# Performance work log

Measured on AMD Instinct MI355X. Metric: run time of the kernel, lower is better.

The kernel has to match this reference:

```python
import jax, jax.numpy as jnp
import numpy as np

B, N, F_IN, F_OUT = 8, 8192, 128, 128
E = 1_048_576
BN = B * N


def setup_inputs() -> dict:
    key = jax.random.key(0)
    ks = jax.random.split(key, 9)
    glorot = (6.0 / (F_IN + F_OUT)) ** 0.5
    return {
        "X": jax.random.normal(ks[0], (B, N, F_IN), dtype=jnp.float32),
        "W0": jax.random.uniform(ks[1], (F_IN, F_OUT), jnp.float32, -glorot, glorot),
        "W1": jax.random.uniform(ks[2], (F_IN, F_OUT), jnp.float32, -glorot, glorot),
        "rows0": jax.random.randint(ks[3], (E,), 0, BN, dtype=jnp.int32),
        "cols0": jax.random.randint(ks[4], (E,), 0, BN, dtype=jnp.int32),
        "vals0": jax.random.uniform(ks[5], (E,), dtype=jnp.float32),
        "rows1": jax.random.randint(ks[6], (E,), 0, BN, dtype=jnp.int32),
        "cols1": jax.random.randint(ks[7], (E,), 0, BN, dtype=jnp.int32),
        "vals1": jax.random.uniform(ks[8], (E,), dtype=jnp.float32),
    }


def _spmm(rows, cols, vals, H, n):
    # COO sparse [n, n] @ dense H [n, F]: gather source rows, scale, scatter-add.
    return jax.ops.segment_sum(vals[:, None] * H[cols], rows, num_segments=n)


def reference(X, W0, W1, rows0, cols0, vals0, rows1, cols1, vals1):
    b, n, f_in = X.shape
    X2 = X.reshape(-1, f_in)                      # [B*N, F_in]
    h0 = _spmm(rows0, cols0, vals0, X2 @ W0, b * n)  # filter_0 @ (X W0)
    h1 = _spmm(rows1, cols1, vals1, X2 @ W1, b * n)  # filter_1 @ (X W1)
    out = jax.nn.relu(h0 + h1).reshape(b, n, -1)  # add_n + relu
    return out
```

## Files before the change

kernel.cpp:

```cpp
#include <hip/hip_runtime.h>


typedef unsigned int   uint;
typedef unsigned short ushort;
typedef unsigned char  uchar;
typedef float f32x4 __attribute__((ext_vector_type(4)));
typedef int   i32x4 __attribute__((ext_vector_type(4)));

constexpr int NB  = 256;
constexpr int EPB = 8192;
constexpr int CAP = 8192;

__device__ __forceinline__ ushort f2bf(float f) {
    uint u = __float_as_uint(f);
    u += 0x7fffu + ((u >> 16) & 1u);
    return (ushort)(u >> 16);
}
__device__ __forceinline__ float bf2f(ushort h) {
    return __uint_as_float((uint)h << 16);
}

#define ACC_FENCE(a) asm volatile("s_nop 7\n\ts_nop 7" : "+v"(a))

__global__ __launch_bounds__(64) void w_swz(const float* __restrict__ W0,
                                            const float* __restrict__ W1,
                                            uint4* __restrict__ Wswz) {
    const int bx = blockIdx.x;
    const int f  = bx >> 5;
    const int ct = (bx >> 2) & 7;
    const int kt = bx & 3;
    const int l  = threadIdx.x;
    const float* W = f ? W1 : W0;
    const int kbase = kt * 32 + (l >> 4) * 8;
    const int col   = ct * 16 + (l & 15);
    ushort h[8];
#pragma unroll
    for (int j = 0; j < 8; ++j)
        h[j] = f2bf(W[(kbase + j) * 128 + col]);
    uint4 o;
    o.x = (uint)h[0] | ((uint)h[1] << 16);
    o.y = (uint)h[2] | ((uint)h[3] << 16);
    o.z = (uint)h[4] | ((uint)h[5] << 16);
    o.w = (uint)h[6] | ((uint)h[7] << 16);
    Wswz[((f * 8 + ct) * 4 + kt) * 64 + l] = o;
}

__global__ __launch_bounds__(256) void gemm_mfma(const float* __restrict__ X,
                                                 const i32x4* __restrict__ Wswz,
                                                 ushort* __restrict__ H, int BN) {
    __shared__ ushort xs_hi[64][136];
    __shared__ ushort xs_lo[64][136];
    const int tid = threadIdx.x;
    const int l = tid & 63;
    const int w = tid >> 6;
    const long rbase = (long)blockIdx.x * 64;

    const float4* Xv = reinterpret_cast<const float4*>(X + rbase * 128);
#pragma unroll
    for (int i = 0; i < 8; ++i) {
        int idx = i * 256 + tid;
        int row = idx >> 5, c4 = idx & 31;
        float4 v = Xv[idx];
        ushort4 hi, lo;
        hi.x = f2bf(v.x); lo.x = f2bf(v.x - bf2f(hi.x));
        hi.y = f2bf(v.y); lo.y = f2bf(v.y - bf2f(hi.y));
        hi.z = f2bf(v.z); lo.z = f2bf(v.z - bf2f(hi.z));
        hi.w = f2bf(v.w); lo.w = f2bf(v.w - bf2f(hi.w));
        *reinterpret_cast<ushort4*>(&xs_hi[row][c4 * 4]) = hi;
        *reinterpret_cast<ushort4*>(&xs_lo[row][c4 * 4]) = lo;
    }
    __syncthreads();

    i32x4 a_hi[4], a_lo[4];
    const int arow = w * 16 + (l & 15);
    const int kb = (l >> 4) * 8;
#pragma unroll
    for (int kt = 0; kt < 4; ++kt) {
        a_hi[kt] = *reinterpret_cast<const i32x4*>(&xs_hi[arow][kt * 32 + kb]);
        a_lo[kt] = *reinterpret_cast<const i32x4*>(&xs_lo[arow][kt * 32 + kb]);
    }

    f32x4 acc[2][8];
#pragma unroll
    for (int f = 0; f < 2; ++f)
#pragma unroll
        for (int ct = 0; ct < 8; ++ct)
            acc[f][ct] = (f32x4)0.0f;

#pragma unroll
    for (int ct = 0; ct < 8; ++ct)
#pragma unroll
        for (int f = 0; f < 2; ++f)
#pragma unroll
            for (int kt = 0; kt < 4; ++kt) {
                i32x4 b = Wswz[((f * 8 + ct) * 4 + kt) * 64 + l];
                asm volatile("v_mfma_f32_16x16x32_bf16 %0, %1, %2, %0"
                             : "+v"(acc[f][ct]) : "v"(a_hi[kt]), "v"(b));
                asm volatile("v_mfma_f32_16x16x32_bf16 %0, %1, %2, %0"
                             : "+v"(acc[f][ct]) : "v"(a_lo[kt]), "v"(b));
            }

#pragma unroll
    for (int ct = 0; ct < 8; ++ct)
#pragma unroll
        for (int f = 0; f < 2; ++f) {
            f32x4 a = acc[f][ct];
            ACC_FENCE(a);
            ushort* Hf = H + (size_t)f * BN * 128;
            size_t base = (size_t)(rbase + w * 16 + (l >> 4) * 4) * 128
                        + ct * 16 + (l & 15);
            Hf[base]       = f2bf(a.x);
            Hf[base + 128] = f2bf(a.y);
            Hf[base + 256] = f2bf(a.z);
            Hf[base + 384] = f2bf(a.w);
        }
}

__global__ __launch_bounds__(256) void hist_coarse(const int* __restrict__ r0,
                                                   const int* __restrict__ r1,
                                                   int* __restrict__ cnt, int E) {
    __shared__ int h[NB];
    const int f = blockIdx.y, t = threadIdx.x;
    const int* rows = f ? r1 : r0;
    h[t] = 0;
    __syncthreads();
    const int base = blockIdx.x * EPB;
    for (int k = 0; k < EPB / 256; ++k) {
        int e = base + k * 256 + t;
        if (e < E) atomicAdd(&h[rows[e] >> 8], 1);
    }
    __syncthreads();
    if (h[t]) atomicAdd(&cnt[f * NB + t], h[t]);
}

__global__ __launch_bounds__(256) void scan_coarse(const int* __restrict__ cnt,
                                                   int* __restrict__ bbase,
                                                   int* __restrict__ bcur) {
    __shared__ int s[NB];
    const int f = blockIdx.x, t = threadIdx.x;
    int v = cnt[f * NB + t];
    s[t] = v;
    __syncthreads();
    for (int off = 1; off < NB; off <<= 1) {
        int u = (t >= off) ? s[t - off] : 0;
        __syncthreads();
        s[t] += u;
        __syncthreads();
    }
    int base = s[t] - v;
    bbase[f * NB + t] = base;
    bcur [f * NB + t] = base;
}

__global__ __launch_bounds__(256) void partition(const int* __restrict__ r0,
                                                 const int* __restrict__ c0,
                                                 const float* __restrict__ v0,
                                                 const int* __restrict__ r1,
                                                 const int* __restrict__ c1,
                                                 const float* __restrict__ v1,
                                                 int* __restrict__ bcur,
                                                 uint* __restrict__ cvy,
                                                 uchar* __restrict__ cvr, int E) {
    __shared__ int h[NB];
    __shared__ int cur[NB];
    const int f = blockIdx.y, t = threadIdx.x;
    const int*   rows = f ? r1 : r0;
    const int*   cols = f ? c1 : c0;
    const float* vals = f ? v1 : v0;
    const int base = blockIdx.x * EPB;

    h[t] = 0;
    __syncthreads();
    for (int k = 0; k < EPB / 256; ++k) {
        int e = base + k * 256 + t;
        if (e < E) atomicAdd(&h[rows[e] >> 8], 1);
    }
    __syncthreads();
    cur[t] = atomicAdd(&bcur[f * NB + t], h[t]);
    __syncthreads();

    uint*  yout = cvy + (size_t)f * E;
    uchar* rout = cvr + (size_t)f * E;
    for (int k = 0; k < EPB / 256; ++k) {
        int e = base + k * 256 + t;
        if (e < E) {
            int r = rows[e];
            int pos = atomicAdd(&cur[r >> 8], 1);
            yout[pos] = ((uint)cols[e] << 16) | (uint)f2bf(vals[e]);
            rout[pos] = (uchar)(r & 255);
        }
    }
}

__device__ __forceinline__ void fma4(float4& a, float v, ushort4 h) {
    a.x = fmaf(v, bf2f(h.x), a.x);
    a.y = fmaf(v, bf2f(h.y), a.y);
    a.z = fmaf(v, bf2f(h.z), a.z);
    a.w = fmaf(v, bf2f(h.w), a.w);
}

__global__ __launch_bounds__(1024) void sort_gather(
        const uint* __restrict__ cvy, const uchar* __restrict__ cvr,
        const int* __restrict__ bbase, const int* __restrict__ bcur,
        const ushort* __restrict__ H, int BN,
        float* __restrict__ out, int E) {
    __shared__ uint cvl[2][CAP];
    __shared__ int rp[2][NB + 1];
    __shared__ int hcnt[NB];
    __shared__ int curs[NB];
    __shared__ int sstart[2], scount[2], sovf[2];

    const int b = blockIdx.x;
    const int t = threadIdx.x;

#pragma unroll 1
    for (int f = 0; f < 2; ++f) {
        if (t == 0) {
            int s0 = bbase[f * NB + b];
            int e0 = bcur [f * NB + b];
            sstart[f] = s0;
            scount[f] = e0 - s0;
            sovf[f]   = (e0 - s0) > CAP;
        }
        if (t < NB) hcnt[t] = 0;
        __syncthreads();
        const int s = sstart[f], n = scount[f];
        const uchar* rin = cvr + (size_t)f * E + s;
        const uint*  yin = cvy + (size_t)f * E + s;
        for (int i = t; i < n; i += 1024)
            atomicAdd(&hcnt[rin[i]], 1);
        __syncthreads();
        int v = (t < NB) ? hcnt[t] : 0;
        if (t < NB) curs[t] = v;
        __syncthreads();
        for (int off = 1; off < NB; off <<= 1) {
            int u = 0;
            if (t < NB && t >= off) u = curs[t - off];
            __syncthreads();
            if (t < NB) curs[t] += u;
            __syncthreads();
        }
        if (t < NB) {
            int ex = curs[t] - v;
            rp[f][t] = ex;
            curs[t] = ex;
        }
        if (t == 0) rp[f][NB] = n;
        __syncthreads();
        if (!sovf[f]) {
            for (int i = t; i < n; i += 1024) {
                uchar r = rin[i];
                int pos = atomicAdd(&curs[r], 1);
                cvl[f][pos] = __builtin_nontemporal_load(&yin[i]);
            }
        }
        __syncthreads();
    }

    const int half = t >> 5;
    const int sub  = t & 31;
    f32x4* outv = reinterpret_cast<f32x4*>(out);

#pragma unroll 1
    for (int k = 0; k < 8; ++k) {
        const int lr = k * 32 + half;
        const long gr = (long)b * NB + lr;

        float4 a0 = make_float4(0.f, 0.f, 0.f, 0.f);
        float4 a1 = make_float4(0.f, 0.f, 0.f, 0.f);
        float4 a2 = make_float4(0.f, 0.f, 0.f, 0.f);
        float4 a3 = make_float4(0.f, 0.f, 0.f, 0.f);

#pragma unroll
        for (int f = 0; f < 2; ++f) {
            const ushort* Hf = H + (size_t)f * BN * 128;
            if (!sovf[f]) {
                int e = rp[f][lr];
                const int e1 = rp[f][lr + 1];
                for (; e + 7 < e1; e += 8) {
                    uint p0 = cvl[f][e],     p1 = cvl[f][e + 1];
                    uint p2 = cvl[f][e + 2], p3 = cvl[f][e + 3];
                    uint p4 = cvl[f][e + 4], p5 = cvl[f][e + 5];
                    uint p6 = cvl[f][e + 6], p7 = cvl[f][e + 7];
                    ushort4 h0 = reinterpret_cast<const ushort4*>(Hf + (size_t)(p0 >> 16) * 128)[sub];
                    ushort4 h1 = reinterpret_cast<const ushort4*>(Hf + (size_t)(p1 >> 16) * 128)[sub];
                    ushort4 h2 = reinterpret_cast<const ushort4*>(Hf + (size_t)(p2 >> 16) * 128)[sub];
                    ushort4 h3 = reinterpret_cast<const ushort4*>(Hf + (size_t)(p3 >> 16) * 128)[sub];
                    ushort4 h4 = reinterpret_cast<const ushort4*>(Hf + (size_t)(p4 >> 16) * 128)[sub];
                    ushort4 h5 = reinterpret_cast<const ushort4*>(Hf + (size_t)(p5 >> 16) * 128)[sub];
                    ushort4 h6 = reinterpret_cast<const ushort4*>(Hf + (size_t)(p6 >> 16) * 128)[sub];
                    ushort4 h7 = reinterpret_cast<const ushort4*>(Hf + (size_t)(p7 >> 16) * 128)[sub];
                    fma4(a0, __uint_as_float(p0 << 16), h0);
                    fma4(a1, __uint_as_float(p1 << 16), h1);
                    fma4(a2, __uint_as_float(p2 << 16), h2);
                    fma4(a3, __uint_as_float(p3 << 16), h3);
                    fma4(a0, __uint_as_float(p4 << 16), h4);
                    fma4(a1, __uint_as_float(p5 << 16), h5);
                    fma4(a2, __uint_as_float(p6 << 16), h6);
                    fma4(a3, __uint_as_float(p7 << 16), h7);
                }
                for (; e + 3 < e1; e += 4) {
                    uint p0 = cvl[f][e],     p1 = cvl[f][e + 1];
                    uint p2 = cvl[f][e + 2], p3 = cvl[f][e + 3];
                    ushort4 h0 = reinterpret_cast<const ushort4*>(Hf + (size_t)(p0 >> 16) * 128)[sub];
                    ushort4 h1 = reinterpret_cast<const ushort4*>(Hf + (size_t)(p1 >> 16) * 128)[sub];
                    ushort4 h2 = reinterpret_cast<const ushort4*>(Hf + (size_t)(p2 >> 16) * 128)[sub];
                    ushort4 h3 = reinterpret_cast<const ushort4*>(Hf + (size_t)(p3 >> 16) * 128)[sub];
                    fma4(a0, __uint_as_float(p0 << 16), h0);
                    fma4(a1, __uint_as_float(p1 << 16), h1);
                    fma4(a2, __uint_as_float(p2 << 16), h2);
                    fma4(a3, __uint_as_float(p3 << 16), h3);
                }
                for (; e < e1; ++e) {
                    uint p0 = cvl[f][e];
                    ushort4 h0 = reinterpret_cast<const ushort4*>(Hf + (size_t)(p0 >> 16) * 128)[sub];
                    fma4(a0, __uint_as_float(p0 << 16), h0);
                }
            } else {
                const int s = sstart[f], n = scount[f];
                const uchar* rin = cvr + (size_t)f * E + s;
                const uint*  yin = cvy + (size_t)f * E + s;
                for (int i = 0; i < n; ++i) {
                    if (rin[i] == (uchar)lr) {
                        uint p0 = yin[i];
                        ushort4 h0 = reinterpret_cast<const ushort4*>(Hf + (size_t)(p0 >> 16) * 128)[sub];
                        fma4(a0, __uint_as_float(p0 << 16), h0);
                    }
                }
            }
        }

        f32x4 o;
        o.x = fmaxf((a0.x + a1.x) + (a2.x + a3.x), 0.0f);
        o.y = fmaxf((a0.y + a1.y) + (a2.y + a3.y), 0.0f);
        o.z = fmaxf((a0.z + a1.z) + (a2.z + a3.z), 0.0f);
        o.w = fmaxf((a0.w + a1.w) + (a2.w + a3.w), 0.0f);
        __builtin_nontemporal_store(o, outv + gr * 32 + sub);
    }
}

extern "C" void kernel_launch(void* const* d_in, const int* in_sizes, int n_in,
                              void* d_out, int out_size, void* d_ws, size_t ws_size,
                              hipStream_t stream) {
    const float* X     = (const float*)d_in[0];
    const float* W0    = (const float*)d_in[1];
    const float* W1    = (const float*)d_in[2];
    const int*   rows0 = (const int*)d_in[3];
    const int*   cols0 = (const int*)d_in[4];
    const float* vals0 = (const float*)d_in[5];
    const int*   rows1 = (const int*)d_in[6];
    const int*   cols1 = (const int*)d_in[7];
    const float* vals1 = (const float*)d_in[8];
    float* out = (float*)d_out;

    const int BN = in_sizes[0] / 128;
    const int E  = in_sizes[3];
    const int partb = (E + EPB - 1) / EPB;

    char* ws = (char*)d_ws;
    size_t off = 0;
    auto alloc = [&](size_t bytes) {
        void* p = ws + off;
        off = (off + bytes + 255) & ~(size_t)255;
        return p;
    };
    ushort* H     = (ushort*)alloc((size_t)2 * BN * 128 * sizeof(ushort));
    uint4*  Wswz  = (uint4*) alloc((size_t)2 * 128 * 128 * sizeof(ushort));
    uint*   cvy   = (uint*)  alloc((size_t)2 * E * sizeof(uint));
    uchar*  cvr   = (uchar*) alloc((size_t)2 * E * sizeof(uchar));
    int*    cnt   = (int*)   alloc((size_t)2 * NB * sizeof(int));
    int*    bbase = (int*)   alloc((size_t)2 * NB * sizeof(int));
    int*    bcur  = (int*)   alloc((size_t)2 * NB * sizeof(int));

    w_swz<<<64, 64, 0, stream>>>(W0, W1, Wswz);
    gemm_mfma<<<BN / 64, 256, 0, stream>>>(X, (const i32x4*)Wswz, H, BN);

    hipMemsetAsync(cnt, 0, (size_t)2 * NB * sizeof(int), stream);
    hist_coarse<<<dim3(partb, 2), 256, 0, stream>>>(rows0, rows1, cnt, E);
    scan_coarse<<<2, 256, 0, stream>>>(cnt, bbase, bcur);
    partition<<<dim3(partb, 2), 256, 0, stream>>>(rows0, cols0, vals0,
                                                  rows1, cols1, vals1,
                                                  bcur, cvy, cvr, E);
    sort_gather<<<NB, 1024, 0, stream>>>(cvy, cvr, bbase, bcur, H, BN, out, E);
}
```

Before: 166.9 us.

## Double coarse buckets to 512, shrink per-block LDS, fold counter zeroing into w_swz

Splits rows into 512 coarse buckets of 128 rows instead of 256 buckets of 256 rows. The sort_gather kernel then runs 512 blocks with a smaller LDS edge buffer, aiming for more blocks in flight and better occupancy across CUs. Partition blocks now process 16384 edges each, and the histogram memset is folded into an extra block of the w_swz kernel to save one launch. The risk is that CAP=3072 sits close to the expected ~2048 edges per bucket, so any overflow drops to the slow path.

Result: slower. 202.3 us, median of 2 (+21.2%).

```diff
diff --git a/kernel.cpp b/kernel.cpp
--- a/kernel.cpp
+++ b/kernel.cpp
@@ -7,9 +7,10 @@
 typedef float f32x4 __attribute__((ext_vector_type(4)));
 typedef int   i32x4 __attribute__((ext_vector_type(4)));
 
-constexpr int NB  = 256;
-constexpr int EPB = 8192;
-constexpr int CAP = 8192;
+constexpr int NBK = 512;
+constexpr int RPB = 128;
+constexpr int EPB = 16384;
+constexpr int CAP = 3072;
 
 __device__ __forceinline__ ushort f2bf(float f) {
     uint u = __float_as_uint(f);
@@ -24,12 +25,17 @@
 
 __global__ __launch_bounds__(64) void w_swz(const float* __restrict__ W0,
                                             const float* __restrict__ W1,
-                                            uint4* __restrict__ Wswz) {
+                                            uint4* __restrict__ Wswz,
+                                            int* __restrict__ cnt) {
     const int bx = blockIdx.x;
+    const int l  = threadIdx.x;
+    if (bx == 64) {
+        for (int i = l; i < 2 * NBK; i += 64) cnt[i] = 0;
+        return;
+    }
     const int f  = bx >> 5;
     const int ct = (bx >> 2) & 7;
     const int kt = bx & 3;
-    const int l  = threadIdx.x;
     const float* W = f ? W1 : W0;
     const int kbase = kt * 32 + (l >> 4) * 8;
     const int col   = ct * 16 + (l & 15);
@@ -119,37 +125,38 @@
 __global__ __launch_bounds__(256) void hist_coarse(const int* __restrict__ r0,
                                                    const int* __restrict__ r1,
                                                    int* __restrict__ cnt, int E) {
-    __shared__ int h[NB];
+    __shared__ int h[NBK];
     const int f = blockIdx.y, t = threadIdx.x;
     const int* rows = f ? r1 : r0;
-    h[t] = 0;
+    for (int i = t; i < NBK; i += 256) h[i] = 0;
     __syncthreads();
     const int base = blockIdx.x * EPB;
     for (int k = 0; k < EPB / 256; ++k) {
         int e = base + k * 256 + t;
-        if (e < E) atomicAdd(&h[rows[e] >> 8], 1);
-    }
-    __syncthreads();
-    if (h[t]) atomicAdd(&cnt[f * NB + t], h[t]);
-}
-
-__global__ __launch_bounds__(256) void scan_coarse(const int* __restrict__ cnt,
+        if (e < E) atomicAdd(&h[rows[e] >> 7], 1);
+    }
+    __syncthreads();
+    for (int i = t; i < NBK; i += 256)
+        if (h[i]) atomicAdd(&cnt[f * NBK + i], h[i]);
+}
+
+__global__ __launch_bounds__(512) void scan_coarse(const int* __restrict__ cnt,
                                                    int* __restrict__ bbase,
                                                    int* __restrict__ bcur) {
-    __shared__ int s[NB];
+    __shared__ int s[NBK];
     const int f = blockIdx.x, t = threadIdx.x;
-    int v = cnt[f * NB + t];
+    int v = cnt[f * NBK + t];
     s[t] = v;
     __syncthreads();
-    for (int off = 1; off < NB; off <<= 1) {
+    for (int off = 1; off < NBK; off <<= 1) {
         int u = (t >= off) ? s[t - off] : 0;
         __syncthreads();
         s[t] += u;
         __syncthreads();
     }
     int base = s[t] - v;
-    bbase[f * NB + t] = base;
-    bcur [f * NB + t] = base;
+    bbase[f * NBK + t] = base;
+    bcur [f * NBK + t] = base;
 }
 
 __global__ __launch_bounds__(256) void partition(const int* __restrict__ r0,
@@ -161,22 +168,23 @@
                                                  int* __restrict__ bcur,
                                                  uint* __restrict__ cvy,
                                                  uchar* __restrict__ cvr, int E) {
-    __shared__ int h[NB];
-    __shared__ int cur[NB];
+    __shared__ int h[NBK];
+    __shared__ int cur[NBK];
     const int f = blockIdx.y, t = threadIdx.x;
     const int*   rows = f ? r1 : r0;
     const int*   cols = f ? c1 : c0;
     const float* vals = f ? v1 : v0;
     const int base = blockIdx.x * EPB;
 
-    h[t] = 0;
+    for (int i = t; i < NBK; i += 256) h[i] = 0;
     __syncthreads();
     for (int k = 0; k < EPB / 256; ++k) {
         int e = base + k * 256 + t;
-        if (e < E) atomicAdd(&h[rows[e] >> 8], 1);
-    }
-    __syncthreads();
-    cur[t] = atomicAdd(&bcur[f * NB + t], h[t]);
+        if (e < E) atomicAdd(&h[rows[e] >> 7], 1);
+    }
+    __syncthreads();
+    for (int i = t; i < NBK; i += 256)
+        cur[i] = atomicAdd(&bcur[f * NBK + i], h[i]);
     __syncthreads();
 
     uint*  yout = cvy + (size_t)f * E;
@@ -185,9 +193,9 @@
         int e = base + k * 256 + t;
         if (e < E) {
             int r = rows[e];
-            int pos = atomicAdd(&cur[r >> 8], 1);
+            int pos = atomicAdd(&cur[r >> 7], 1);
             yout[pos] = ((uint)cols[e] << 16) | (uint)f2bf(vals[e]);
-            rout[pos] = (uchar)(r & 255);
+            rout[pos] = (uchar)(r & 127);
         }
     }
 }
@@ -205,9 +213,9 @@
         const ushort* __restrict__ H, int BN,
         float* __restrict__ out, int E) {
     __shared__ uint cvl[2][CAP];
-    __shared__ int rp[2][NB + 1];
-    __shared__ int hcnt[NB];
-    __shared__ int curs[NB];
+    __shared__ int rp[2][RPB + 1];
+    __shared__ int hcnt[RPB];
+    __shared__ int curs[RPB];
     __shared__ int sstart[2], scount[2], sovf[2];
 
     const int b = blockIdx.x;
@@ -216,13 +224,13 @@
 #pragma unroll 1
     for (int f = 0; f < 2; ++f) {
         if (t == 0) {
-            int s0 = bbase[f * NB + b];
-            int e0 = bcur [f * NB + b];
+            int s0 = bbase[f * NBK + b];
+            int e0 = bcur [f * NBK + b];
             sstart[f] = s0;
             scount[f] = e0 - s0;
             sovf[f]   = (e0 - s0) > CAP;
         }
-        if (t < NB) hcnt[t] = 0;
+        if (t < RPB) hcnt[t] = 0;
         __syncthreads();
         const int s = sstart[f], n = scount[f];
         const uchar* rin = cvr + (size_t)f * E + s;
@@ -230,22 +238,22 @@
         for (int i = t; i < n; i += 1024)
             atomicAdd(&hcnt[rin[i]], 1);
         __syncthreads();
-        int v = (t < NB) ? hcnt[t] : 0;
-        if (t < NB) curs[t] = v;
-        __syncthreads();
-        for (int off = 1; off < NB; off <<= 1) {
+        int v = (t < RPB) ? hcnt[t] : 0;
+        if (t < RPB) curs[t] = v;
+        __syncthreads();
+        for (int off = 1; off < RPB; off <<= 1) {
             int u = 0;
-            if (t < NB && t >= off) u = curs[t - off];
+            if (t < RPB && t >= off) u = curs[t - off];
             __syncthreads();
-            if (t < NB) curs[t] += u;
+            if (t < RPB) curs[t] += u;
             __syncthreads();
         }
-        if (t < NB) {
+        if (t < RPB) {
             int ex = curs[t] - v;
             rp[f][t] = ex;
             curs[t] = ex;
         }
-        if (t == 0) rp[f][NB] = n;
+        if (t == 0) rp[f][RPB] = n;
         __syncthreads();
         if (!sovf[f]) {
             for (int i = t; i < n; i += 1024) {
@@ -262,9 +270,9 @@
     f32x4* outv = reinterpret_cast<f32x4*>(out);
 
 #pragma unroll 1
-    for (int k = 0; k < 8; ++k) {
+    for (int k = 0; k < 4; ++k) {
         const int lr = k * 32 + half;
-        const long gr = (long)b * NB + lr;
+        const long gr = (long)b * RPB + lr;
 
         float4 a0 = make_float4(0.f, 0.f, 0.f, 0.f);
         float4 a1 = make_float4(0.f, 0.f, 0.f, 0.f);
@@ -368,18 +376,17 @@
     uint4*  Wswz  = (uint4*) alloc((size_t)2 * 128 * 128 * sizeof(ushort));
     uint*   cvy   = (uint*)  alloc((size_t)2 * E * sizeof(uint));
     uchar*  cvr   = (uchar*) alloc((size_t)2 * E * sizeof(uchar));
-    int*    cnt   = (int*)   alloc((size_t)2 * NB * sizeof(int));
-    int*    bbase = (int*)   alloc((size_t)2 * NB * sizeof(int));
-    int*    bcur  = (int*)   alloc((size_t)2 * NB * sizeof(int));
-
-    w_swz<<<64, 64, 0, stream>>>(W0, W1, Wswz);
+    int*    cnt   = (int*)   alloc((size_t)2 * NBK * sizeof(int));
+    int*    bbase = (int*)   alloc((size_t)2 * NBK * sizeof(int));
+    int*    bcur  = (int*)   alloc((size_t)2 * NBK * sizeof(int));
+
+    w_swz<<<65, 64, 0, stream>>>(W0, W1, Wswz, cnt);
     gemm_mfma<<<BN / 64, 256, 0, stream>>>(X, (const i32x4*)Wswz, H, BN);
 
-    hipMemsetAsync(cnt, 0, (size_t)2 * NB * sizeof(int), stream);
     hist_coarse<<<dim3(partb, 2), 256, 0, stream>>>(rows0, rows1, cnt, E);
-    scan_coarse<<<2, 256, 0, stream>>>(cnt, bbase, bcur);
+    scan_coarse<<<2, 512, 0, stream>>>(cnt, bbase, bcur);
     partition<<<dim3(partb, 2), 256, 0, stream>>>(rows0, cols0, vals0,
                                                   rows1, cols1, vals1,
                                                   bcur, cvy, cvr, E);
-    sort_gather<<<NB, 1024, 0, stream>>>(cvy, cvr, bbase, bcur, H, BN, out, E);
-}
+    sort_gather<<<NBK, 1024, 0, stream>>>(cvy, cvr, bbase, bcur, H, BN, out, E);
+}
```
